# Kernel tuning notes

Hardware: AMD Instinct MI355X
Metric: run time of the kernel (lower is better)

Reference implementation:

```python
import jax, jax.numpy as jnp
import numpy as np


def setup_inputs() -> dict:
    key = jax.random.key(0)
    k1, k2, k3, k4 = jax.random.split(key, 4)
    B, Q, D, H = 8, 512, 4096, 1024
    return {
        "query_embeddings": jax.random.normal(k1, (B, Q, H), dtype=jnp.float32),
        "document_embeddings": jax.random.normal(k2, (B, D, H), dtype=jnp.float32),
        "attention_mask": jax.random.randint(k3, (B, D), 0, 2, dtype=jnp.int32),
        "proj_w": jax.random.normal(k4, (H, H), dtype=jnp.float32) * (H ** -0.5),
        "proj_b": jnp.zeros((H,), dtype=jnp.float32),
    }


def reference(query_embeddings, document_embeddings, attention_mask, proj_w, proj_b):
    H = query_embeddings.shape[-1]
    scale = 1.0 / jnp.sqrt(jnp.asarray(H, dtype=query_embeddings.dtype))
    # Linear projection of queries: [B, Q, H]
    q = jnp.einsum("bqh,hk->bqk", query_embeddings, proj_w) + proj_b
    # Scores: [B, Q, D]
    scores = jnp.einsum("bqh,bdh->bqd", q, document_embeddings) * scale
    # Mask: [B, 1, D]; masked positions -> -inf before softmax
    mask = attention_mask[:, None, :] != 0
    scores = jnp.where(mask, scores, -jnp.inf)
    attention_weights = jax.nn.softmax(scores, axis=-1)
    # Weighted sum over docs: [B, Q, H]
    retrieved_docs = jnp.einsum("bqd,bdh->bqh", attention_weights, document_embeddings)
    return (retrieved_docs, attention_weights)
```

## Files before the change

kernel.cpp:

```cpp
#include <hip/hip_runtime.h>

#define BATCH 8
#define QLEN 512
#define DLEN 4096
#define HDIM 1024

typedef __attribute__((ext_vector_type(8))) short bf16x8;
typedef __attribute__((ext_vector_type(4))) float f32x4;
typedef __attribute__((ext_vector_type(4))) short s16x4;

__device__ __forceinline__ short f2bf(float f) {
    union { float f; unsigned u; } x; x.f = f;
    unsigned r = x.u + 0x7fffu + ((x.u >> 16) & 1u);
    return (short)(r >> 16);
}

__device__ __forceinline__ void gload_lds16(const void* g, void* l) {
    __builtin_amdgcn_global_load_lds(
        (const __attribute__((address_space(1))) unsigned int*)g,
        (__attribute__((address_space(3))) unsigned int*)l,
        16, 0, 0);
}

__global__ void cvt_f32_bf16(const float* __restrict__ in, short* __restrict__ out, int n4) {
    int i = blockIdx.x * blockDim.x + threadIdx.x;
    int stride = gridDim.x * blockDim.x;
    for (; i < n4; i += stride) {
        float4 x = ((const float4*)in)[i];
        s16x4 o = { f2bf(x.x), f2bf(x.y), f2bf(x.z), f2bf(x.w) };
        ((s16x4*)out)[i] = o;
    }
}

__global__ void transpose_w(const float* __restrict__ W, short* __restrict__ Wt) {
    __shared__ float t[32][33];
    const int hb = blockIdx.y * 32, kb = blockIdx.x * 32;
    #pragma unroll
    for (int i = 0; i < 4; ++i) {
        int h = threadIdx.y + i * 8;
        t[h][threadIdx.x] = W[(size_t)(hb + h) * HDIM + kb + threadIdx.x];
    }
    __syncthreads();
    #pragma unroll
    for (int i = 0; i < 4; ++i) {
        int k = threadIdx.y + i * 8;
        Wt[(size_t)(kb + k) * HDIM + hb + threadIdx.x] = f2bf(t[threadIdx.x][k]);
    }
}

__global__ void prep_docs(const float* __restrict__ docs,
                          short* __restrict__ docsB, short* __restrict__ docsT) {
    __shared__ float t[64][65];
    const int b = blockIdx.z;
    const int h0 = blockIdx.x * 64, d0 = blockIdx.y * 64;
    const int tq = threadIdx.x & 15;
    const int tr = threadIdx.x >> 4;
    const float* src = docs + ((size_t)b * DLEN + d0) * HDIM + h0;
    #pragma unroll
    for (int i = 0; i < 4; ++i) {
        int d = tr + i * 16;
        float4 v = *(const float4*)(src + (size_t)d * HDIM + tq * 4);
        t[d][tq * 4 + 0] = v.x;
        t[d][tq * 4 + 1] = v.y;
        t[d][tq * 4 + 2] = v.z;
        t[d][tq * 4 + 3] = v.w;
        s16x4 o = { f2bf(v.x), f2bf(v.y), f2bf(v.z), f2bf(v.w) };
        *(s16x4*)(docsB + ((size_t)b * DLEN + d0 + d) * HDIM + h0 + tq * 4) = o;
    }
    __syncthreads();
    #pragma unroll
    for (int i = 0; i < 4; ++i) {
        int h = tr + i * 16;
        s16x4 o = { f2bf(t[tq * 4 + 0][h]), f2bf(t[tq * 4 + 1][h]),
                    f2bf(t[tq * 4 + 2][h]), f2bf(t[tq * 4 + 3][h]) };
        *(s16x4*)(docsT + ((size_t)b * HDIM + h0 + h) * DLEN + d0 + tq * 4) = o;
    }
}

#define BM 128
#define BN 128
#define BK 64

template<int EPI>
__global__ void gemm_bt(const short* __restrict__ A, const short* __restrict__ B,
                        void* __restrict__ Cv, const float* __restrict__ bias,
                        float scale, int N, int Kstride, int Kloop, int kOffStep,
                        long long aB, long long bB, long long cB) {
    __shared__ short As[BM * BK];
    __shared__ short Bs[BN * BK];
    const int tid  = threadIdx.x;
    const int lane = tid & 63;
    const int wv   = tid >> 6;
    const int wr   = wv >> 1, wc = wv & 1;
    const size_t rowBase = (size_t)blockIdx.y * BM;
    const size_t colBase = (size_t)blockIdx.x * BN;
    const int z = blockIdx.z;
    const int bb = z & 7;
    const int kOff = (z >> 3) * kOffStep;
    const short* Ag = A + (size_t)bb * aB + kOff;
    const short* Bg = B + (size_t)bb * bB + kOff;

    f32x4 acc[4][4];
    #pragma unroll
    for (int m = 0; m < 4; ++m)
        #pragma unroll
        for (int n = 0; n < 4; ++n)
            acc[m][n] = (f32x4){0.f, 0.f, 0.f, 0.f};

    const short* aSrc[4]; const short* bSrc[4]; short* aDst[4]; short* bDst[4];
    #pragma unroll
    for (int i = 0; i < 4; ++i) {
        const int c = tid + 256 * i;
        const int r = c >> 3, cc = c & 7;
        const int gk = (cc ^ (r & 7)) << 3;
        aSrc[i] = Ag + (rowBase + r) * (size_t)Kstride + gk;
        bSrc[i] = Bg + (colBase + r) * (size_t)Kstride + gk;
        aDst[i] = As + c * 8;
        bDst[i] = Bs + c * 8;
    }
    const int lr = lane & 15;
    const int lk = (lane >> 4) << 3;

    for (int kt = 0; kt < Kloop; kt += BK) {
        #pragma unroll
        for (int i = 0; i < 4; ++i) gload_lds16(aSrc[i] + kt, aDst[i]);
        #pragma unroll
        for (int i = 0; i < 4; ++i) gload_lds16(bSrc[i] + kt, bDst[i]);
        __syncthreads();

        #pragma unroll
        for (int kk = 0; kk < 2; ++kk) {
            const int chunkL = (kk * 32 + lk) >> 3;
            bf16x8 af[4], bfr[4];
            #pragma unroll
            for (int m = 0; m < 4; ++m) {
                const int row = wr * 64 + m * 16 + lr;
                af[m] = *(const bf16x8*)(As + row * BK + ((chunkL ^ (row & 7)) << 3));
            }
            #pragma unroll
            for (int n = 0; n < 4; ++n) {
                const int row = wc * 64 + n * 16 + lr;
                bfr[n] = *(const bf16x8*)(Bs + row * BK + ((chunkL ^ (row & 7)) << 3));
            }
            #pragma unroll
            for (int m = 0; m < 4; ++m)
                #pragma unroll
                for (int n = 0; n < 4; ++n)
                    acc[m][n] = __builtin_amdgcn_mfma_f32_16x16x32_bf16(af[m], bfr[n], acc[m][n], 0, 0, 0);
        }
        __syncthreads();
    }

    const int orow = (lane >> 4) << 2;
    const int ocol = lane & 15;
    #pragma unroll
    for (int n = 0; n < 4; ++n) {
        const size_t col = colBase + wc * 64 + n * 16 + ocol;
        const float bv = (EPI == 0) ? bias[col] : 0.f;
        #pragma unroll
        for (int m = 0; m < 4; ++m) {
            const size_t rbase = rowBase + wr * 64 + m * 16 + orow;
            #pragma unroll
            for (int j = 0; j < 4; ++j) {
                const float v = acc[m][n][j];
                const size_t off = (size_t)z * cB + (rbase + j) * (size_t)N + col;
                if (EPI == 0)      ((short*)Cv)[off] = f2bf(v + bv);
                else if (EPI == 1) ((float*)Cv)[off] = v * scale;
                else               ((float*)Cv)[off] = v;
            }
        }
    }
}

__global__ void reduce4(const float* __restrict__ p, float* __restrict__ out, int n4) {
    int i = blockIdx.x * blockDim.x + threadIdx.x;
    const int stride = gridDim.x * blockDim.x;
    const float4* p4 = (const float4*)p;
    float4* o4 = (float4*)out;
    for (; i < n4; i += stride) {
        float4 a = p4[i];
        float4 b = p4[i + 1048576];
        float4 c = p4[i + 2097152];
        float4 d = p4[i + 3145728];
        float4 r;
        r.x = a.x + b.x + c.x + d.x;
        r.y = a.y + b.y + c.y + d.y;
        r.z = a.z + b.z + c.z + d.z;
        r.w = a.w + b.w + c.w + d.w;
        o4[i] = r;
    }
}

__global__ void softmax_rows(const float* __restrict__ scores, const int* __restrict__ mask,
                             float* __restrict__ attnF, short* __restrict__ attnB) {
    const int row = blockIdx.x;
    const int b   = row >> 9;
    const int tid = threadIdx.x;
    const int lane = tid & 63;
    const int wv = tid >> 6;
    const float4* S  = (const float4*)(scores + (size_t)row * DLEN);
    const int4*   Mk = (const int4*)(mask + (size_t)b * DLEN);
    __shared__ float red[8];

    float v[16];
    float mx = -INFINITY;
    #pragma unroll
    for (int i = 0; i < 4; ++i) {
        float4 s = S[i * 256 + tid];
        int4   m = Mk[i * 256 + tid];
        v[i * 4 + 0] = m.x ? s.x : -INFINITY;
        v[i * 4 + 1] = m.y ? s.y : -INFINITY;
        v[i * 4 + 2] = m.z ? s.z : -INFINITY;
        v[i * 4 + 3] = m.w ? s.w : -INFINITY;
        #pragma unroll
        for (int c = 0; c < 4; ++c) mx = fmaxf(mx, v[i * 4 + c]);
    }
    #pragma unroll
    for (int o = 32; o > 0; o >>= 1) mx = fmaxf(mx, __shfl_xor(mx, o));
    if (lane == 0) red[wv] = mx;
    __syncthreads();
    mx = fmaxf(fmaxf(red[0], red[1]), fmaxf(red[2], red[3]));

    float sum = 0.f;
    #pragma unroll
    for (int i = 0; i < 16; ++i) {
        float e = __expf(v[i] - mx);
        v[i] = e;
        sum += e;
    }
    #pragma unroll
    for (int o = 32; o > 0; o >>= 1) sum += __shfl_xor(sum, o);
    __syncthreads();
    if (lane == 0) red[4 + wv] = sum;
    __syncthreads();
    sum = red[4] + red[5] + red[6] + red[7];
    const float inv = 1.0f / sum;

    float4* OF = (float4*)(attnF + (size_t)row * DLEN);
    s16x4*  OB = (s16x4*)(attnB + (size_t)row * DLEN);
    #pragma unroll
    for (int i = 0; i < 4; ++i) {
        float4 w;
        w.x = v[i * 4 + 0] * inv;
        w.y = v[i * 4 + 1] * inv;
        w.z = v[i * 4 + 2] * inv;
        w.w = v[i * 4 + 3] * inv;
        OF[i * 256 + tid] = w;
        s16x4 o = { f2bf(w.x), f2bf(w.y), f2bf(w.z), f2bf(w.w) };
        OB[i * 256 + tid] = o;
    }
}

extern "C" void kernel_launch(void* const* d_in, const int* in_sizes, int n_in,
                              void* d_out, int out_size, void* d_ws, size_t ws_size,
                              hipStream_t stream) {
    const float* qe   = (const float*)d_in[0];
    const float* docs = (const float*)d_in[1];
    const int*   mask = (const int*)d_in[2];
    const float* pw   = (const float*)d_in[3];
    const float* pb   = (const float*)d_in[4];

    float* outRet  = (float*)d_out;
    float* outAttn = outRet + (size_t)BATCH * QLEN * HDIM;

    char* ws = (char*)d_ws;
    short* qeB   = (short*)(ws + 0);
    short* wt    = (short*)(ws + 8388608);
    short* qpB   = (short*)(ws + 10485760);
    short* docsB = (short*)(ws + 18874368);
    short* docsT = (short*)(ws + 85983232);
    float* scor  = (float*)(ws + 153092096);
    short* attnB = (short*)(ws + 220200960);

    cvt_f32_bf16<<<dim3(1024), dim3(256), 0, stream>>>(qe, qeB, (BATCH * QLEN * HDIM) / 4);
    transpose_w<<<dim3(32, 32), dim3(32, 8), 0, stream>>>(pw, wt);
    prep_docs<<<dim3(HDIM / 64, DLEN / 64, BATCH), dim3(256), 0, stream>>>(docs, docsB, docsT);

    gemm_bt<0><<<dim3(HDIM / BN, (BATCH * QLEN) / BM, 1), dim3(256), 0, stream>>>(
        qeB, wt, (void*)qpB, pb, 1.f, HDIM, HDIM, HDIM, 0,
        0LL, 0LL, 0LL);

    gemm_bt<1><<<dim3(DLEN / BN, QLEN / BM, BATCH), dim3(256), 0, stream>>>(
        qpB, docsB, (void*)scor, nullptr, 0.03125f, DLEN, HDIM, HDIM, 0,
        (long long)QLEN * HDIM, (long long)DLEN * HDIM, (long long)QLEN * DLEN);

    softmax_rows<<<dim3(BATCH * QLEN), dim3(256), 0, stream>>>(scor, mask, outAttn, attnB);

    gemm_bt<2><<<dim3(HDIM / BN, QLEN / BM, BATCH * 4), dim3(256), 0, stream>>>(
        attnB, docsT, (void*)scor, nullptr, 1.f, HDIM, DLEN, DLEN / 4, DLEN / 4,
        (long long)QLEN * DLEN, (long long)HDIM * DLEN, (long long)QLEN * HDIM);

    reduce4<<<dim3(2048), dim3(256), 0, stream>>>(scor, outRet, (BATCH * QLEN * HDIM) / 4);
}
```

Baseline: 434.2 us.

## Remap GEMM workgroups to 1D grid with XCD-aware swizzle; split doc prep

The three GEMM launches now use a flat 1D grid. Each workgroup index is permuted so that consecutive tiles sharing A/B panels land on the same XCD (blockIdx mod 8 interleave), which should improve L2 reuse across the chiplets. The fused docs conversion+transpose kernel is split into a plain f32->bf16 conversion followed by a bf16 transpose that reads the converted buffer. This reads fewer bytes in the transpose but adds an extra pass over the bf16 docs.

```diff
diff --git a/kernel.cpp b/kernel.cpp
--- a/kernel.cpp
+++ b/kernel.cpp
@@ -48,31 +48,27 @@
     }
 }
 
-__global__ void prep_docs(const float* __restrict__ docs,
-                          short* __restrict__ docsB, short* __restrict__ docsT) {
-    __shared__ float t[64][65];
+__global__ void transpose_docs(const short* __restrict__ docsB, short* __restrict__ docsT) {
+    __shared__ unsigned t[64][65];
     const int b = blockIdx.z;
     const int h0 = blockIdx.x * 64, d0 = blockIdx.y * 64;
     const int tq = threadIdx.x & 15;
     const int tr = threadIdx.x >> 4;
-    const float* src = docs + ((size_t)b * DLEN + d0) * HDIM + h0;
     #pragma unroll
     for (int i = 0; i < 4; ++i) {
         int d = tr + i * 16;
-        float4 v = *(const float4*)(src + (size_t)d * HDIM + tq * 4);
-        t[d][tq * 4 + 0] = v.x;
-        t[d][tq * 4 + 1] = v.y;
-        t[d][tq * 4 + 2] = v.z;
-        t[d][tq * 4 + 3] = v.w;
-        s16x4 o = { f2bf(v.x), f2bf(v.y), f2bf(v.z), f2bf(v.w) };
-        *(s16x4*)(docsB + ((size_t)b * DLEN + d0 + d) * HDIM + h0 + tq * 4) = o;
+        s16x4 v = *(const s16x4*)(docsB + ((size_t)b * DLEN + d0 + d) * HDIM + h0 + tq * 4);
+        t[d][tq * 4 + 0] = (unsigned short)v[0];
+        t[d][tq * 4 + 1] = (unsigned short)v[1];
+        t[d][tq * 4 + 2] = (unsigned short)v[2];
+        t[d][tq * 4 + 3] = (unsigned short)v[3];
     }
     __syncthreads();
     #pragma unroll
     for (int i = 0; i < 4; ++i) {
         int h = tr + i * 16;
-        s16x4 o = { f2bf(t[tq * 4 + 0][h]), f2bf(t[tq * 4 + 1][h]),
-                    f2bf(t[tq * 4 + 2][h]), f2bf(t[tq * 4 + 3][h]) };
+        s16x4 o = { (short)t[tq * 4 + 0][h], (short)t[tq * 4 + 1][h],
+                    (short)t[tq * 4 + 2][h], (short)t[tq * 4 + 3][h] };
         *(s16x4*)(docsT + ((size_t)b * HDIM + h0 + h) * DLEN + d0 + tq * 4) = o;
     }
 }
@@ -85,6 +81,7 @@
 __global__ void gemm_bt(const short* __restrict__ A, const short* __restrict__ B,
                         void* __restrict__ Cv, const float* __restrict__ bias,
                         float scale, int N, int Kstride, int Kloop, int kOffStep,
+                        int sx, int sxy,
                         long long aB, long long bB, long long cB) {
     __shared__ short As[BM * BK];
     __shared__ short Bs[BN * BK];
@@ -92,9 +89,14 @@
     const int lane = tid & 63;
     const int wv   = tid >> 6;
     const int wr   = wv >> 1, wc = wv & 1;
-    const size_t rowBase = (size_t)blockIdx.y * BM;
-    const size_t colBase = (size_t)blockIdx.x * BN;
-    const int z = blockIdx.z;
+
+    const int wg = (blockIdx.x & 7) * (gridDim.x >> 3) + (blockIdx.x >> 3);
+    const int bx = wg & ((1 << sx) - 1);
+    const int by = (wg >> sx) & ((1 << (sxy - sx)) - 1);
+    const int z  = wg >> sxy;
+
+    const size_t rowBase = (size_t)by * BM;
+    const size_t colBase = (size_t)bx * BN;
     const int bb = z & 7;
     const int kOff = (z >> 3) * kOffStep;
     const short* Ag = A + (size_t)bb * aB + kOff;
@@ -273,21 +275,22 @@
     short* attnB = (short*)(ws + 220200960);
 
     cvt_f32_bf16<<<dim3(1024), dim3(256), 0, stream>>>(qe, qeB, (BATCH * QLEN * HDIM) / 4);
+    cvt_f32_bf16<<<dim3(2048), dim3(256), 0, stream>>>(docs, docsB, (BATCH * DLEN * HDIM) / 4);
     transpose_w<<<dim3(32, 32), dim3(32, 8), 0, stream>>>(pw, wt);
-    prep_docs<<<dim3(HDIM / 64, DLEN / 64, BATCH), dim3(256), 0, stream>>>(docs, docsB, docsT);
-
-    gemm_bt<0><<<dim3(HDIM / BN, (BATCH * QLEN) / BM, 1), dim3(256), 0, stream>>>(
-        qeB, wt, (void*)qpB, pb, 1.f, HDIM, HDIM, HDIM, 0,
+    transpose_docs<<<dim3(HDIM / 64, DLEN / 64, BATCH), dim3(256), 0, stream>>>(docsB, docsT);
+
+    gemm_bt<0><<<dim3(256), dim3(256), 0, stream>>>(
+        qeB, wt, (void*)qpB, pb, 1.f, HDIM, HDIM, HDIM, 0, 3, 8,
         0LL, 0LL, 0LL);
 
-    gemm_bt<1><<<dim3(DLEN / BN, QLEN / BM, BATCH), dim3(256), 0, stream>>>(
-        qpB, docsB, (void*)scor, nullptr, 0.03125f, DLEN, HDIM, HDIM, 0,
+    gemm_bt<1><<<dim3(1024), dim3(256), 0, stream>>>(
+        qpB, docsB, (void*)scor, nullptr, 0.03125f, DLEN, HDIM, HDIM, 0, 5, 7,
         (long long)QLEN * HDIM, (long long)DLEN * HDIM, (long long)QLEN * DLEN);
 
     softmax_rows<<<dim3(BATCH * QLEN), dim3(256), 0, stream>>>(scor, mask, outAttn, attnB);
 
-    gemm_bt<2><<<dim3(HDIM / BN, QLEN / BM, BATCH * 4), dim3(256), 0, stream>>>(
-        attnB, docsT, (void*)scor, nullptr, 1.f, HDIM, DLEN, DLEN / 4, DLEN / 4,
+    gemm_bt<2><<<dim3(1024), dim3(256), 0, stream>>>(
+        attnB, docsT, (void*)scor, nullptr, 1.f, HDIM, DLEN, DLEN / 4, DLEN / 4, 3, 5,
         (long long)QLEN * DLEN, (long long)HDIM * DLEN, (long long)QLEN * HDIM);
 
     reduce4<<<dim3(2048), dim3(256), 0, stream>>>(scor, outRet, (BATCH * QLEN * HDIM) / 4);
```

After: 414.4 us. -4.6%, faster.
